# Optimization experiments

Measured on AMD Instinct MI355X. Metric: run time of the kernel, lower is better.

## Reference

```python
import jax, jax.numpy as jnp
import numpy as np

# Model constants (match init_kwargs)
H = 256          # hidden_dim
NH = 4           # num_heads
L = 4            # gnn_layers
T = 4            # transformer_layers
KMAX = 10        # k_max for overlap embedding
MAXD = 32        # MAX_DIST
INC = 119        # in_channels (atom vocab)
ED = 5           # edge_dim (bond vocab)
B = 64           # graphs per batch
M_SUB = 32       # subgraphs per graph (m)
KNODE = 32       # nodes per subgraph (k)
S = B * M_SUB    # total subgraphs = 2048
N = S * KNODE    # flattened nodes = 65536
E = 131072       # intra-subgraph directed edges


def _ln(x, g, b):
    mu = x.mean(-1, keepdims=True)
    var = ((x - mu) ** 2).mean(-1, keepdims=True)
    return (x - mu) * jax.lax.rsqrt(var + 1e-5) * g + b


def setup_inputs() -> dict:
    key = jax.random.key(0)
    ks = iter(jax.random.split(key, 24))
    nk = lambda: next(ks)
    rn = lambda k_, shp: 0.02 * jax.random.normal(k_, shp, dtype=jnp.float32)

    x_ids = jax.random.randint(nk(), (N,), 0, INC)
    edge_ids = jax.random.randint(nk(), (E,), 0, ED)
    # intra-subgraph edges: endpoints stay within each block of KNODE nodes
    eps_per = E // S
    base = jnp.repeat(jnp.arange(S) * KNODE, eps_per)
    src = base + jax.random.randint(nk(), (E,), 0, KNODE)
    dst = base + jax.random.randint(nk(), (E,), 0, KNODE)
    ns = jax.random.randint(nk(), (S, KNODE), 0, 500)
    padm = jax.random.uniform(nk(), (S, KNODE)) < 0.1
    nodes_sampled = jnp.where(padm, -1, ns)
    dist = jax.random.randint(nk(), (N,), 0, MAXD + 1)
    lp = -5.0 * jax.random.uniform(nk(), (S,))

    return {
        'x_ids': x_ids, 'edge_ids': edge_ids, 'src': src, 'dst': dst,
        'nodes_sampled': nodes_sampled, 'dist': dist, 'lp': lp,
        'atom_emb': rn(nk(), (INC, H)), 'bond_emb': rn(nk(), (ED, H)),
        'dist_emb': rn(nk(), (MAXD + 1, H)),
        'logp_W': rn(nk(), (H,)), 'logp_b': jnp.zeros((H,)),
        'gnn_eps': jnp.zeros((L,)),
        'gnn_W1': rn(nk(), (L, H, H)), 'gnn_b1': jnp.zeros((L, H)),
        'gnn_W2': rn(nk(), (L, H, H)), 'gnn_b2': jnp.zeros((L, H)),
        'ln1_g': jnp.ones((T, H)), 'ln1_b': jnp.zeros((T, H)),
        'qkv_W': rn(nk(), (T, H, 3 * H)),
        'out_W': rn(nk(), (T, H, H)), 'out_b': jnp.zeros((T, H)),
        'ln2_g': jnp.ones((T, H)), 'ln2_b': jnp.zeros((T, H)),
        'f1_W': rn(nk(), (T, H, 4 * H)), 'f1_b': jnp.zeros((T, 4 * H)),
        'f2_W': rn(nk(), (T, 4 * H, H)), 'f2_b': jnp.zeros((T, H)),
        'lnout_g': jnp.ones((H,)), 'lnout_b': jnp.zeros((H,)),
        'overlap_emb': rn(nk(), (KMAX + 1,)),
        'ht_alpha': jnp.ones(()),
    }


def reference(x_ids, edge_ids, src, dst, nodes_sampled, dist, lp,
              atom_emb, bond_emb, dist_emb, logp_W, logp_b,
              gnn_eps, gnn_W1, gnn_b1, gnn_W2, gnn_b2,
              ln1_g, ln1_b, qkv_W, out_W, out_b, ln2_g, ln2_b,
              f1_W, f1_b, f2_W, f2_b, lnout_g, lnout_b,
              overlap_emb, ht_alpha):
    # ---- flatten / embed node features ----
    valid = (nodes_sampled >= 0).reshape(N)
    valid_f = valid.astype(jnp.float32)[:, None]
    lp = jnp.where(jnp.isfinite(lp), lp, 0.0)
    sub_batch = jnp.arange(N) // KNODE
    dist_c = jnp.clip(dist, 0, MAXD)
    logp_pe = jax.nn.relu(lp[sub_batch][:, None] * logp_W + logp_b)
    h = (atom_emb[x_ids] + dist_emb[dist_c] + logp_pe) * valid_f  # [N,H]
    e = bond_emb[edge_ids]                                        # [E,H]

    # ---- GINE message passing ----
    for l in range(L):
        msg = jax.nn.relu(h[src] + e)                       # [E,H] gather
        agg = jax.ops.segment_sum(msg, dst, num_segments=N) # [N,H] scatter-add
        z = (1.0 + gnn_eps[l]) * h + agg
        z = jax.nn.relu(z @ gnn_W1[l] + gnn_b1[l])
        h = (z @ gnn_W2[l] + gnn_b2[l]) * valid_f

    # ---- pool roots into [B, m, H] tokens ----
    root = jnp.arange(S) * KNODE
    x = h[root].reshape(B, M_SUB, H)
    lp2 = lp.reshape(B, M_SUB)

    # ---- pairwise subgraph overlap bias ----
    nodes = nodes_sampled.reshape(B, M_SUB, KNODE)
    vmask = nodes >= 0
    # eq[b,i,j,ki,kj]: node ki of subgraph i equals node kj of subgraph j
    eq = nodes[:, :, None, :, None] == nodes[:, None, :, None, :]
    overlap = (eq.any(-1) & vmask[:, :, None, :]).sum(-1)  # [B,m,m]
    lp_c = jnp.clip(lp2, -30.0, 0.0)
    bias = overlap_emb[jnp.clip(overlap, 0, KMAX)] - ht_alpha * lp_c[:, None, :]
    bias = bias[:, None]  # [B,1,m,m], broadcast over heads

    # ---- relative-bias transformer ----
    hd = H // NH
    scale = 1.0 / np.sqrt(hd).astype(np.float32)
    for t in range(T):
        r = _ln(x, ln1_g[t], ln1_b[t])
        q, k_, v = jnp.split(r @ qkv_W[t], 3, axis=-1)
        q = q.reshape(B, M_SUB, NH, hd)
        k_ = k_.reshape(B, M_SUB, NH, hd)
        v = v.reshape(B, M_SUB, NH, hd)
        scores = jnp.einsum('bihd,bjhd->bhij', q, k_) * scale + bias
        attn = jax.nn.softmax(scores, axis=-1)
        o = jnp.einsum('bhij,bjhd->bihd', attn, v).reshape(B, M_SUB, H)
        x = x + o @ out_W[t] + out_b[t]
        r2 = _ln(x, ln2_g[t], ln2_b[t])
        x = x + jax.nn.gelu(r2 @ f1_W[t] + f1_b[t], approximate=False) @ f2_W[t] + f2_b[t]

    x = _ln(x, lnout_g, lnout_b)
    # HT-weighted mean over subgraph tokens
    w = jax.nn.softmax(-lp_c, axis=1)
    return (w[:, :, None] * x).sum(1)  # [B,H]
```

## Files before the change

kernel.cpp:

```cpp
#include <hip/hip_runtime.h>
#include <hip/hip_bf16.h>
#include <math.h>

#define HDIM   256
#define NHEAD  4
#define LLAY   4
#define TLAY   4
#define KMAXC  10
#define MAXD   32
#define BATCH  64
#define MSUB   32
#define KNODE  32
#define SSUB   2048
#define NNODE  65536
#define NEDGE  131072
#define EPSPER 64
#define EDN    5

typedef unsigned short u16;
typedef __attribute__((ext_vector_type(8))) short bf16x8;
typedef __attribute__((ext_vector_type(4))) float f32x4;

__device__ __forceinline__ float us2f(u16 u) {
    union { unsigned int i; float f; } x; x.i = ((unsigned int)u) << 16; return x.f;
}
__device__ __forceinline__ u16 f2us(float v) {
    union { float f; unsigned int i; } x; x.f = v;
    unsigned int u = x.i;
    u += 0x7fffu + ((u >> 16) & 1u);
    return (u16)(u >> 16);
}
__device__ __forceinline__ float finite_or_zero(float v) {
    return (v == v && fabsf(v) <= 3.0e38f) ? v : 0.0f;
}
__device__ __forceinline__ void gll16(const u16* g, u16* l) {
    __builtin_amdgcn_global_load_lds(
        (const __attribute__((address_space(1))) unsigned int*)g,
        (__attribute__((address_space(3))) unsigned int*)l, 16, 0, 0);
}

__global__ __launch_bounds__(256) void k_csr(
    const int* __restrict__ src, const int* __restrict__ dst,
    const int* __restrict__ eid, u16* __restrict__ perm, u16* __restrict__ off)
{
    __shared__ int sL[4][64], dL[4][64], eL[4][64];
    int wave = threadIdx.x >> 6, lane = threadIdx.x & 63;
    int sgi = blockIdx.x * 4 + wave;
    sL[wave][lane] = src[sgi * 64 + lane] - sgi * KNODE;
    dL[wave][lane] = dst[sgi * 64 + lane] - sgi * KNODE;
    eL[wave][lane] = eid[sgi * 64 + lane];
    __syncthreads();
    if (lane < 32) {
        int cnt = 0;
        for (int e = 0; e < 64; ++e) cnt += (dL[wave][e] == lane) ? 1 : 0;
        int incl = cnt;
        #pragma unroll
        for (int d = 1; d < 32; d <<= 1) {
            int v = __shfl_up(incl, d, 64);
            if (lane >= d) incl += v;
        }
        int start = incl - cnt;
        off[sgi * 32 + lane] = (u16)start;
        int pos = start;
        for (int e = 0; e < 64; ++e) {
            if (dL[wave][e] == lane) {
                perm[sgi * 64 + pos] = (u16)((sL[wave][e] << 3) | eL[wave][e]);
                ++pos;
            }
        }
    }
}

__global__ __launch_bounds__(256) void k_wtrans(
    const float* __restrict__ W, u16* __restrict__ WT, int K, int N)
{
    __shared__ float til[32][33];
    int k0 = blockIdx.x * 32, n0 = blockIdx.y * 32, s = blockIdx.z;
    const float* Wb = W + (size_t)s * K * N;
    u16* Tb = WT + (size_t)s * N * K;
    int j = threadIdx.x & 31, i0 = threadIdx.x >> 5;
    #pragma unroll
    for (int it = 0; it < 4; ++it) {
        int i = i0 + it * 8;
        til[i][j] = Wb[(size_t)(k0 + i) * N + n0 + j];
    }
    __syncthreads();
    #pragma unroll
    for (int it = 0; it < 4; ++it) {
        int i = i0 + it * 8;
        Tb[(size_t)(n0 + i) * K + k0 + j] = f2us(til[j][i]);
    }
}

__global__ __launch_bounds__(256, 4) void k_gnn4(
    const int* __restrict__ x_ids, const int* __restrict__ dist,
    const int* __restrict__ nodes, const float* __restrict__ lp,
    const float* __restrict__ atom_emb, const float* __restrict__ dist_emb,
    const float* __restrict__ logp_W, const float* __restrict__ logp_b,
    const u16* __restrict__ perm, const u16* __restrict__ off,
    const float* __restrict__ bond_emb, const float* __restrict__ eps_arr,
    const float* __restrict__ b1a, const float* __restrict__ b2a,
    const u16* __restrict__ W1T, const u16* __restrict__ W2T,
    float* __restrict__ x)
{
    __shared__ __align__(16) unsigned char smem[38912];
    u16*   hz    = (u16*)smem;
    float* bondL = (float*)(smem + 32768);
    u16*   permL = (u16*)(smem + 32768 + 5120);
    u16*   offL  = (u16*)(smem + 32768 + 5120 + 256);
    float* validL= (float*)(smem + 32768 + 5120 + 512);
    float* epsL  = (float*)(smem + 32768 + 5120 + 512 + 256);

    int tid = threadIdx.x, lane = tid & 63, wave = tid >> 6;
    int row0 = blockIdx.x * 64;
    int fr = lane & 15, quad = lane >> 4;

    for (int i = tid; i < EDN * 256; i += 256) bondL[i] = bond_emb[i];
    if (tid < 128) permL[tid] = perm[blockIdx.x * 128 + tid];
    if (tid < 64) {
        offL[tid] = off[blockIdx.x * 64 + tid];
        validL[tid] = (nodes[row0 + tid] >= 0) ? 1.0f : 0.0f;
    }
    if (tid < 4) epsL[tid] = eps_arr[tid];

    {
        int m = tid & 63, qd = tid >> 6;
        int rg = row0 + m;
        float valid = (nodes[rg] >= 0) ? 1.0f : 0.0f;
        float lpv = finite_or_zero(lp[rg >> 5]);
        int dc = dist[rg]; dc = dc < 0 ? 0 : (dc > MAXD ? MAXD : dc);
        int xid = x_ids[rg];
        #pragma unroll
        for (int k = 0; k < 8; ++k) {
            int cc = qd * 8 + k, c = cc * 8;
            float4 a0 = *reinterpret_cast<const float4*>(atom_emb + xid * 256 + c);
            float4 a1 = *reinterpret_cast<const float4*>(atom_emb + xid * 256 + c + 4);
            float4 d0 = *reinterpret_cast<const float4*>(dist_emb + dc * 256 + c);
            float4 d1 = *reinterpret_cast<const float4*>(dist_emb + dc * 256 + c + 4);
            float4 w0 = *reinterpret_cast<const float4*>(logp_W + c);
            float4 w1 = *reinterpret_cast<const float4*>(logp_W + c + 4);
            float4 p0 = *reinterpret_cast<const float4*>(logp_b + c);
            float4 p1 = *reinterpret_cast<const float4*>(logp_b + c + 4);
            union { bf16x8 v; ushort4 h[2]; } o;
            o.h[0] = (ushort4){
                f2us((a0.x + d0.x + fmaxf(lpv * w0.x + p0.x, 0.f)) * valid),
                f2us((a0.y + d0.y + fmaxf(lpv * w0.y + p0.y, 0.f)) * valid),
                f2us((a0.z + d0.z + fmaxf(lpv * w0.z + p0.z, 0.f)) * valid),
                f2us((a0.w + d0.w + fmaxf(lpv * w0.w + p0.w, 0.f)) * valid) };
            o.h[1] = (ushort4){
                f2us((a1.x + d1.x + fmaxf(lpv * w1.x + p1.x, 0.f)) * valid),
                f2us((a1.y + d1.y + fmaxf(lpv * w1.y + p1.y, 0.f)) * valid),
                f2us((a1.z + d1.z + fmaxf(lpv * w1.z + p1.z, 0.f)) * valid),
                f2us((a1.w + d1.w + fmaxf(lpv * w1.w + p1.w, 0.f)) * valid) };
            *reinterpret_cast<bf16x8*>(hz + m * 256 + ((cc ^ (m & 7)) * 8)) = o.v;
        }
    }
    __syncthreads();

    int rl = tid >> 3, g8 = tid & 7;
    for (int l = 0; l < LLAY; ++l) {
        float ep1 = 1.0f + epsL[l];
        for (int p = 0; p < 2; ++p) {
            int row = p * 32 + rl;
            int e0 = offL[p * 32 + rl];
            int e1 = (rl < 31) ? offL[p * 32 + rl + 1] : 64;
            float a[32];
            #pragma unroll
            for (int q = 0; q < 32; ++q) a[q] = 0.f;
            for (int j = e0; j < e1; ++j) {
                int ent = permL[p * 64 + j];
                int sl = p * 32 + (ent >> 3);
                int be = ent & 7;
                #pragma unroll
                for (int q = 0; q < 4; ++q) {
                    union { bf16x8 v; u16 s[8]; } hv;
                    hv.v = *reinterpret_cast<const bf16x8*>(
                        hz + sl * 256 + (((g8 * 4 + q) ^ (sl & 7)) * 8));
                    const float* bp = bondL + be * 256 + g8 * 32 + q * 8;
                    float4 bo0 = *reinterpret_cast<const float4*>(bp);
                    float4 bo1 = *reinterpret_cast<const float4*>(bp + 4);
                    a[q*8+0] += fmaxf(us2f(hv.s[0]) + bo0.x, 0.f);
                    a[q*8+1] += fmaxf(us2f(hv.s[1]) + bo0.y, 0.f);
                    a[q*8+2] += fmaxf(us2f(hv.s[2]) + bo0.z, 0.f);
                    a[q*8+3] += fmaxf(us2f(hv.s[3]) + bo0.w, 0.f);
                    a[q*8+4] += fmaxf(us2f(hv.s[4]) + bo1.x, 0.f);
                    a[q*8+5] += fmaxf(us2f(hv.s[5]) + bo1.y, 0.f);
                    a[q*8+6] += fmaxf(us2f(hv.s[6]) + bo1.z, 0.f);
                    a[q*8+7] += fmaxf(us2f(hv.s[7]) + bo1.w, 0.f);
                }
            }
            __syncthreads();
            #pragma unroll
            for (int q = 0; q < 4; ++q) {
                u16* ptr = hz + row * 256 + (((g8 * 4 + q) ^ (row & 7)) * 8);
                union { bf16x8 v; u16 s[8]; } hv, ov;
                hv.v = *reinterpret_cast<const bf16x8*>(ptr);
                #pragma unroll
                for (int k = 0; k < 8; ++k)
                    ov.s[k] = f2us(ep1 * us2f(hv.s[k]) + a[q * 8 + k]);
                *reinterpret_cast<bf16x8*>(ptr) = ov.v;
            }
        }
        __syncthreads();

        const u16* W1 = W1T + l * 65536;
        const float* b1 = b1a + l * 256;
        bf16x8 wf[4][8];
        #pragma unroll
        for (int i = 0; i < 4; ++i)
            #pragma unroll
            for (int kc = 0; kc < 8; ++kc)
                wf[i][kc] = *reinterpret_cast<const bf16x8*>(
                    W1 + (size_t)(wave * 64 + i * 16 + fr) * 256 + kc * 32 + quad * 8);
        f32x4 acc[4][4];
        #pragma unroll
        for (int i = 0; i < 4; ++i)
            #pragma unroll
            for (int j = 0; j < 4; ++j) acc[i][j] = (f32x4){0.f, 0.f, 0.f, 0.f};
        #pragma unroll
        for (int kc = 0; kc < 8; ++kc) {
            bf16x8 bfv[4];
            #pragma unroll
            for (int j = 0; j < 4; ++j) {
                int m = j * 16 + fr;
                bfv[j] = *reinterpret_cast<const bf16x8*>(hz + m * 256 + (((kc * 4 + quad) ^ (m & 7)) * 8));
            }
            #pragma unroll
            for (int i = 0; i < 4; ++i)
                #pragma unroll
                for (int j = 0; j < 4; ++j)
                    acc[i][j] = __builtin_amdgcn_mfma_f32_16x16x32_bf16(wf[i][kc], bfv[j], acc[i][j], 0, 0, 0);
        }
        __syncthreads();
        #pragma unroll
        for (int i = 0; i < 4; ++i) {
            int n1b = wave * 64 + i * 16 + quad * 4;
            float4 bb = *reinterpret_cast<const float4*>(b1 + n1b);
            #pragma unroll
            for (int j = 0; j < 4; ++j) {
                int m = j * 16 + fr;
                ushort4 o = { f2us(fmaxf(acc[i][j][0] + bb.x, 0.f)),
                              f2us(fmaxf(acc[i][j][1] + bb.y, 0.f)),
                              f2us(fmaxf(acc[i][j][2] + bb.z, 0.f)),
                              f2us(fmaxf(acc[i][j][3] + bb.w, 0.f)) };
                *reinterpret_cast<ushort4*>(hz + m * 256 + (((n1b >> 3) ^ (m & 7)) * 8) + (n1b & 7)) = o;
            }
        }
        __syncthreads();

        const u16* W2 = W2T + l * 65536;
        const float* b2 = b2a + l * 256;
        #pragma unroll
        for (int i = 0; i < 4; ++i)
            #pragma unroll
            for (int kc = 0; kc < 8; ++kc)
                wf[i][kc] = *reinterpret_cast<const bf16x8*>(
                    W2 + (size_t)(wave * 64 + i * 16 + fr) * 256 + kc * 32 + quad * 8);
        #pragma unroll
        for (int i = 0; i < 4; ++i)
            #pragma unroll
            for (int j = 0; j < 4; ++j) acc[i][j] = (f32x4){0.f, 0.f, 0.f, 0.f};
        #pragma unroll
        for (int kc = 0; kc < 8; ++kc) {
            bf16x8 bfv[4];
            #pragma unroll
            for (int j = 0; j < 4; ++j) {
                int m = j * 16 + fr;
                bfv[j] = *reinterpret_cast<const bf16x8*>(hz + m * 256 + (((kc * 4 + quad) ^ (m & 7)) * 8));
            }
            #pragma unroll
            for (int i = 0; i < 4; ++i)
                #pragma unroll
                for (int j = 0; j < 4; ++j)
                    acc[i][j] = __builtin_amdgcn_mfma_f32_16x16x32_bf16(wf[i][kc], bfv[j], acc[i][j], 0, 0, 0);
        }
        __syncthreads();

        if (l < LLAY - 1) {
            #pragma unroll
            for (int i = 0; i < 4; ++i) {
                int n2b = wave * 64 + i * 16 + quad * 4;
                float4 bb = *reinterpret_cast<const float4*>(b2 + n2b);
                #pragma unroll
                for (int j = 0; j < 4; ++j) {
                    int m = j * 16 + fr;
                    float vm = validL[m];
                    ushort4 o = { f2us((acc[i][j][0] + bb.x) * vm),
                                  f2us((acc[i][j][1] + bb.y) * vm),
                                  f2us((acc[i][j][2] + bb.z) * vm),
                                  f2us((acc[i][j][3] + bb.w) * vm) };
                    *reinterpret_cast<ushort4*>(hz + m * 256 + (((n2b >> 3) ^ (m & 7)) * 8) + (n2b & 7)) = o;
                }
            }
            __syncthreads();
        } else {
            if (fr == 0) {
                #pragma unroll
                for (int i = 0; i < 4; ++i) {
                    int n2b = wave * 64 + i * 16 + quad * 4;
                    float4 bb = *reinterpret_cast<const float4*>(b2 + n2b);
                    #pragma unroll
                    for (int jj = 0; jj < 2; ++jj) {
                        int j = jj * 2, m = j * 16;
                        float vm = validL[m];
                        float4 o = { (acc[i][j][0] + bb.x) * vm,
                                     (acc[i][j][1] + bb.y) * vm,
                                     (acc[i][j][2] + bb.z) * vm,
                                     (acc[i][j][3] + bb.w) * vm };
                        *reinterpret_cast<float4*>(
                            x + (size_t)(blockIdx.x * 2 + (m >> 5)) * 256 + n2b) = o;
                    }
                }
            }
        }
    }
}

__global__ __launch_bounds__(256) void k_tgemm64(
    const u16* __restrict__ A, const u16* __restrict__ BT,
    const float* __restrict__ bias, void* __restrict__ Cout, int c_is_bf16,
    const float* __restrict__ resid, const int* __restrict__ valid,
    int M, int K, int N, int act)
{
    __shared__ __align__(16) u16 As[2][64 * 32];
    __shared__ __align__(16) u16 Bs[2][64 * 32];
    int tid = threadIdx.x, lane = tid & 63, wave = tid >> 6;
    int wm = wave >> 1, wn = wave & 1;
    int bm = blockIdx.y * 64, bn = blockIdx.x * 64;
    const u16* gA = A + (size_t)(bm + wave * 16 + (lane >> 2)) * K + (lane & 3) * 8;
    const u16* gB = BT + (size_t)(bn + wave * 16 + (lane >> 2)) * K + (lane & 3) * 8;
    gll16(gA, &As[0][wave * 512]);
    gll16(gB, &Bs[0][wave * 512]);
    f32x4 acc[2][2];
    #pragma unroll
    for (int i = 0; i < 2; ++i)
        #pragma unroll
        for (int j = 0; j < 2; ++j) acc[i][j] = (f32x4){0.f, 0.f, 0.f, 0.f};
    int fr = lane & 15, quad = lane >> 4;
    int nit = K >> 5;
    __syncthreads();
    for (int it = 0; it < nit; ++it) {
        int buf = it & 1;
        if (it + 1 < nit) {
            int k0 = (it + 1) * 32;
            gll16(gA + k0, &As[buf ^ 1][wave * 512]);
            gll16(gB + k0, &Bs[buf ^ 1][wave * 512]);
        }
        bf16x8 af[2], bfr[2];
        #pragma unroll
        for (int i = 0; i < 2; ++i)
            af[i] = *reinterpret_cast<const bf16x8*>(&As[buf][(wm * 32 + i * 16 + fr) * 32 + quad * 8]);
        #pragma unroll
        for (int j = 0; j < 2; ++j)
            bfr[j] = *reinterpret_cast<const bf16x8*>(&Bs[buf][(wn * 32 + j * 16 + fr) * 32 + quad * 8]);
        #pragma unroll
        for (int i = 0; i < 2; ++i)
            #pragma unroll
            for (int j = 0; j < 2; ++j)
                acc[i][j] = __builtin_amdgcn_mfma_f32_16x16x32_bf16(af[i], bfr[j], acc[i][j], 0, 0, 0);
        __syncthreads();
    }
    int crow0 = bm + wm * 32 + quad * 4;
    int ccol0 = bn + wn * 32 + fr;
    #pragma unroll
    for (int i = 0; i < 2; ++i) {
        #pragma unroll
        for (int r = 0; r < 4; ++r) {
            int m = crow0 + i * 16 + r;
            float vm = valid ? ((valid[m] >= 0) ? 1.0f : 0.0f) : 1.0f;
            #pragma unroll
            for (int j = 0; j < 2; ++j) {
                int n = ccol0 + j * 16;
                float v = acc[i][j][r];
                if (bias) v += bias[n];
                if (act == 1) v = v > 0.f ? v : 0.f;
                else if (act == 2) v = 0.5f * v * (1.0f + erff(v * 0.70710678118654752f));
                v *= vm;
                if (resid) v += resid[(size_t)m * N + n];
                if (c_is_bf16) ((u16*)Cout)[(size_t)m * N + n] = f2us(v);
                else ((float*)Cout)[(size_t)m * N + n] = v;
            }
        }
    }
}

__global__ __launch_bounds__(256) void k_ln(
    const float* __restrict__ X, u16* __restrict__ Out,
    const float* __restrict__ g, const float* __restrict__ b)
{
    int row = blockIdx.x * 4 + (threadIdx.x >> 6);
    int lane = threadIdx.x & 63;
    float4 xv = *reinterpret_cast<const float4*>(X + (size_t)row * HDIM + lane * 4);
    float s = xv.x + xv.y + xv.z + xv.w;
    #pragma unroll
    for (int off = 32; off > 0; off >>= 1) s += __shfl_xor(s, off);
    float mu = s * (1.0f / HDIM);
    float d0 = xv.x - mu, d1 = xv.y - mu, d2 = xv.z - mu, d3 = xv.w - mu;
    float sq = d0 * d0 + d1 * d1 + d2 * d2 + d3 * d3;
    #pragma unroll
    for (int off = 32; off > 0; off >>= 1) sq += __shfl_xor(sq, off);
    float rs = rsqrtf(sq * (1.0f / HDIM) + 1e-5f);
    int c = lane * 4;
    float4 gv = *reinterpret_cast<const float4*>(g + c);
    float4 bv = *reinterpret_cast<const float4*>(b + c);
    ushort4 o = { f2us(d0 * rs * gv.x + bv.x), f2us(d1 * rs * gv.y + bv.y),
                  f2us(d2 * rs * gv.z + bv.z), f2us(d3 * rs * gv.w + bv.w) };
    *reinterpret_cast<ushort4*>(Out + (size_t)row * HDIM + c) = o;
}

__global__ __launch_bounds__(1024) void k_bias(
    const int* __restrict__ nodes, const float* __restrict__ lp,
    const float* __restrict__ ovl_emb, const float* __restrict__ alpha_p,
    float* __restrict__ bias)
{
    int b = blockIdx.x, tid = threadIdx.x;
    __shared__ int nd[32][32];
    __shared__ unsigned int bmv[32][17];
    __shared__ float lpc[32];
    __shared__ float emb[16];
    nd[tid >> 5][tid & 31] = nodes[b * 1024 + tid];
    if (tid < 512) bmv[tid >> 4][tid & 15] = 0u;
    if (tid < 32) {
        float l = finite_or_zero(lp[b * 32 + tid]);
        l = l < -30.f ? -30.f : (l > 0.f ? 0.f : l);
        lpc[tid] = l;
    }
    if (tid >= 64 && tid < 64 + KMAXC + 1) emb[tid - 64] = ovl_emb[tid - 64];
    __syncthreads();
    int own = nd[tid >> 5][tid & 31];
    if (own >= 0) atomicOr(&bmv[tid >> 5][own >> 5], 1u << (own & 31));
    __syncthreads();
    int i = tid >> 5, j = tid & 31;
    float alpha = alpha_p[0];
    int cnt = 0;
    #pragma unroll
    for (int k = 0; k < 32; ++k) {
        int nk = nd[i][k];
        if (nk >= 0) cnt += (int)((bmv[j][nk >> 5] >> (nk & 31)) & 1u);
    }
    bias[b * 1024 + tid] = emb[cnt > KMAXC ? KMAXC : cnt] - alpha * lpc[j];
}

__global__ __launch_bounds__(256) void k_attn(
    const u16* __restrict__ qkv, const float* __restrict__ bias, u16* __restrict__ o)
{
    int b = blockIdx.x >> 2, hh = blockIdx.x & 3;
    __shared__ float qs[32][65], ks[32][65], vs[32][65];
    __shared__ float sc[32][33];
    int tid = threadIdx.x;
    #pragma unroll
    for (int u = 0; u < 8; ++u) {
        int idx = tid + u * 256;
        int i = idx >> 6, d = idx & 63;
        size_t base = (size_t)(b * 32 + i) * 768;
        qs[i][d] = us2f(qkv[base + hh * 64 + d]);
        ks[i][d] = us2f(qkv[base + 256 + hh * 64 + d]);
        vs[i][d] = us2f(qkv[base + 512 + hh * 64 + d]);
    }
    __syncthreads();
    #pragma unroll
    for (int u = 0; u < 4; ++u) {
        int p = tid + u * 256;
        int i = p >> 5, j = p & 31;
        float s = 0.f;
        #pragma unroll
        for (int d = 0; d < 64; ++d) s += qs[i][d] * ks[j][d];
        sc[i][j] = s * 0.125f + bias[b * 1024 + i * 32 + j];
    }
    __syncthreads();
    if (tid < 32) {
        int i = tid;
        float m = -1e30f;
        for (int j = 0; j < 32; ++j) m = fmaxf(m, sc[i][j]);
        float sum = 0.f;
        for (int j = 0; j < 32; ++j) { float e = expf(sc[i][j] - m); sc[i][j] = e; sum += e; }
        float inv = 1.0f / sum;
        for (int j = 0; j < 32; ++j) sc[i][j] *= inv;
    }
    __syncthreads();
    #pragma unroll
    for (int u = 0; u < 8; ++u) {
        int idx = tid + u * 256;
        int i = idx >> 6, d = idx & 63;
        float a = 0.f;
        #pragma unroll
        for (int j = 0; j < 32; ++j) a += sc[i][j] * vs[j][d];
        o[(size_t)(b * 32 + i) * HDIM + hh * 64 + d] = f2us(a);
    }
}

__global__ __launch_bounds__(256) void k_final(
    const u16* __restrict__ xln, const float* __restrict__ lp, float* __restrict__ out)
{
    int b = blockIdx.x, tid = threadIdx.x;
    __shared__ float w[32];
    if (tid < 32) {
        float l = finite_or_zero(lp[b * 32 + tid]);
        l = l < -30.f ? -30.f : (l > 0.f ? 0.f : l);
        w[tid] = -l;
    }
    __syncthreads();
    if (tid == 0) {
        float m = -1e30f;
        for (int i = 0; i < 32; ++i) m = fmaxf(m, w[i]);
        float s = 0.f;
        for (int i = 0; i < 32; ++i) { float e = expf(w[i] - m); w[i] = e; s += e; }
        float inv = 1.0f / s;
        for (int i = 0; i < 32; ++i) w[i] *= inv;
    }
    __syncthreads();
    float acc = 0.f;
    for (int i = 0; i < 32; ++i) acc += w[i] * us2f(xln[(size_t)(b * 32 + i) * HDIM + tid]);
    out[b * HDIM + tid] = acc;
}

extern "C" void kernel_launch(void* const* d_in, const int* in_sizes, int n_in,
                              void* d_out, int out_size, void* d_ws, size_t ws_size,
                              hipStream_t stream)
{
    const int*   x_ids    = (const int*)d_in[0];
    const int*   edge_ids = (const int*)d_in[1];
    const int*   srcp     = (const int*)d_in[2];
    const int*   dstp     = (const int*)d_in[3];
    const int*   nodes    = (const int*)d_in[4];
    const int*   dist     = (const int*)d_in[5];
    const float* lp       = (const float*)d_in[6];
    const float* atom_emb = (const float*)d_in[7];
    const float* bond_emb = (const float*)d_in[8];
    const float* dist_emb = (const float*)d_in[9];
    const float* logp_W   = (const float*)d_in[10];
    const float* logp_b   = (const float*)d_in[11];
    const float* gnn_eps  = (const float*)d_in[12];
    const float* gnn_W1   = (const float*)d_in[13];
    const float* gnn_b1   = (const float*)d_in[14];
    const float* gnn_W2   = (const float*)d_in[15];
    const float* gnn_b2   = (const float*)d_in[16];
    const float* ln1_g    = (const float*)d_in[17];
    const float* ln1_b    = (const float*)d_in[18];
    const float* qkv_W    = (const float*)d_in[19];
    const float* out_W    = (const float*)d_in[20];
    const float* out_b    = (const float*)d_in[21];
    const float* ln2_g    = (const float*)d_in[22];
    const float* ln2_b    = (const float*)d_in[23];
    const float* f1_W     = (const float*)d_in[24];
    const float* f1_b     = (const float*)d_in[25];
    const float* f2_W     = (const float*)d_in[26];
    const float* f2_b     = (const float*)d_in[27];
    const float* lnout_g  = (const float*)d_in[28];
    const float* lnout_b  = (const float*)d_in[29];
    const float* ovl_emb  = (const float*)d_in[30];
    const float* alpha    = (const float*)d_in[31];

    char* ws = (char*)d_ws;
    u16*   gW1T  = (u16*)(ws + 100663296ull);
    u16*   gW2T  = (u16*)(ws + 100663296ull + 524288ull);
    u16*   permW = (u16*)(ws + 100663296ull + 1048576ull);
    u16*   offW  = (u16*)(ws + 100663296ull + 1310720ull);
    u16*   r     = (u16*)(ws + 33554432ull);
    u16*   ob    = (u16*)(ws + 33554432ull + 1048576ull);
    u16*   qkvb  = (u16*)(ws + 33554432ull + 2097152ull);
    u16*   ffh   = (u16*)(ws + 33554432ull + 5242880ull);
    u16*   xln   = (u16*)(ws + 33554432ull + 9437184ull);
    float* biasb = (float*)(ws + 33554432ull + 10485760ull);
    u16*   qkvT  = (u16*)(ws + 33554432ull + 11534336ull);
    u16*   outT  = (u16*)(ws + 33554432ull + 13107200ull);
    u16*   f1T   = (u16*)(ws + 33554432ull + 13631488ull);
    u16*   f2T   = (u16*)(ws + 33554432ull + 15728640ull);
    float* x     = (float*)(ws + 67108864ull);

    k_csr<<<SSUB / 4, 256, 0, stream>>>(srcp, dstp, edge_ids, permW, offW);
    k_wtrans<<<dim3(8, 8, 4), 256, 0, stream>>>(gnn_W1, gW1T, 256, 256);
    k_wtrans<<<dim3(8, 8, 4), 256, 0, stream>>>(gnn_W2, gW2T, 256, 256);
    k_gnn4<<<NNODE / 64, 256, 0, stream>>>(
        x_ids, dist, nodes, lp, atom_emb, dist_emb, logp_W, logp_b,
        permW, offW, bond_emb, gnn_eps, gnn_b1, gnn_b2, gW1T, gW2T, x);
    k_wtrans<<<dim3(8, 24, 4), 256, 0, stream>>>(qkv_W, qkvT, 256, 768);
    k_wtrans<<<dim3(8, 8, 4), 256, 0, stream>>>(out_W, outT, 256, 256);
    k_wtrans<<<dim3(8, 32, 4), 256, 0, stream>>>(f1_W, f1T, 256, 1024);
    k_wtrans<<<dim3(32, 8, 4), 256, 0, stream>>>(f2_W, f2T, 1024, 256);
    k_bias<<<BATCH, 1024, 0, stream>>>(nodes, lp, ovl_emb, alpha, biasb);
    for (int t = 0; t < TLAY; ++t) {
        k_ln<<<SSUB / 4, 256, 0, stream>>>(x, r, ln1_g + t * HDIM, ln1_b + t * HDIM);
        k_tgemm64<<<dim3(12, SSUB / 64), 256, 0, stream>>>(
            r, qkvT + t * 768 * 256, nullptr, qkvb, 1,
            nullptr, nullptr, SSUB, 256, 768, 0);
        k_attn<<<BATCH * NHEAD, 256, 0, stream>>>(qkvb, biasb, ob);
        k_tgemm64<<<dim3(4, SSUB / 64), 256, 0, stream>>>(
            ob, outT + t * 65536, out_b + t * HDIM, x, 0,
            x, nullptr, SSUB, 256, HDIM, 0);
        k_ln<<<SSUB / 4, 256, 0, stream>>>(x, r, ln2_g + t * HDIM, ln2_b + t * HDIM);
        k_tgemm64<<<dim3(16, SSUB / 64), 256, 0, stream>>>(
            r, f1T + t * 1024 * 256, f1_b + t * 1024, ffh, 1,
            nullptr, nullptr, SSUB, 256, 1024, 2);
        k_tgemm64<<<dim3(4, SSUB / 64), 256, 0, stream>>>(
            ffh, f2T + t * 256 * 1024, f2_b + t * HDIM, x, 0,
            x, nullptr, SSUB, 1024, HDIM, 0);
    }
    k_ln<<<SSUB / 4, 256, 0, stream>>>(x, xln, lnout_g, lnout_b);
    k_final<<<BATCH, 256, 0, stream>>>(xln, lp, (float*)d_out);
}
```

Baseline: 587.1 us.

## Fuse entire transformer stack into one per-graph persistent kernel

```diff
diff --git a/kernel.cpp b/kernel.cpp
--- a/kernel.cpp
+++ b/kernel.cpp
@@ -92,7 +92,7 @@
     }
 }
 
-__global__ __launch_bounds__(256, 4) void k_gnn4(
+__global__ __launch_bounds__(256, 2) void k_gnn4(
     const int* __restrict__ x_ids, const int* __restrict__ dist,
     const int* __restrict__ nodes, const float* __restrict__ lp,
     const float* __restrict__ atom_emb, const float* __restrict__ dist_emb,
@@ -316,202 +316,387 @@
     }
 }
 
-__global__ __launch_bounds__(256) void k_tgemm64(
-    const u16* __restrict__ A, const u16* __restrict__ BT,
-    const float* __restrict__ bias, void* __restrict__ Cout, int c_is_bf16,
-    const float* __restrict__ resid, const int* __restrict__ valid,
-    int M, int K, int N, int act)
+#define TF_XF    0
+#define TF_RB    33280
+#define TF_BIAS  49664
+#define TF_LPC   53888
+#define TF_WFIN  54016
+#define TF_EMB   54144
+#define TF_U     54272
+#define TF_QKV   54272
+#define TF_QS    103424
+#define TF_KS    111744
+#define TF_VS    120064
+#define TF_SC    128384
+#define TF_OB    132608
+#define TF_FFH   54272
+#define TF_XLN   54272
+#define XSTR 260
+__global__ __launch_bounds__(256, 1) void k_tformer(
+    const float* __restrict__ x, const int* __restrict__ nodes,
+    const float* __restrict__ lp, const float* __restrict__ ovl_emb,
+    const float* __restrict__ alpha_p,
+    const float* __restrict__ ln1_g, const float* __restrict__ ln1_b,
+    const u16* __restrict__ qkvT, const u16* __restrict__ outT,
+    const float* __restrict__ out_b,
+    const float* __restrict__ ln2_g, const float* __restrict__ ln2_b,
+    const u16* __restrict__ f1T, const float* __restrict__ f1_b,
+    const u16* __restrict__ f2T, const float* __restrict__ f2_b,
+    const float* __restrict__ lnout_g, const float* __restrict__ lnout_b,
+    float* __restrict__ out)
 {
-    __shared__ __align__(16) u16 As[2][64 * 32];
-    __shared__ __align__(16) u16 Bs[2][64 * 32];
+    __shared__ __align__(16) unsigned char smem[148992];
+    float* xf   = (float*)(smem + TF_XF);
+    u16*   rb   = (u16*)(smem + TF_RB);
+    float* biasL= (float*)(smem + TF_BIAS);
+    float* lpc  = (float*)(smem + TF_LPC);
+    float* wfin = (float*)(smem + TF_WFIN);
+    float* emb  = (float*)(smem + TF_EMB);
+    u16*   qkvb = (u16*)(smem + TF_QKV);
+    float* qs   = (float*)(smem + TF_QS);
+    float* ks   = (float*)(smem + TF_KS);
+    float* vs   = (float*)(smem + TF_VS);
+    float* sc   = (float*)(smem + TF_SC);
+    u16*   obL  = (u16*)(smem + TF_OB);
+    u16*   ffh  = (u16*)(smem + TF_FFH);
+    float* xlnf = (float*)(smem + TF_XLN);
+
     int tid = threadIdx.x, lane = tid & 63, wave = tid >> 6;
-    int wm = wave >> 1, wn = wave & 1;
-    int bm = blockIdx.y * 64, bn = blockIdx.x * 64;
-    const u16* gA = A + (size_t)(bm + wave * 16 + (lane >> 2)) * K + (lane & 3) * 8;
-    const u16* gB = BT + (size_t)(bn + wave * 16 + (lane >> 2)) * K + (lane & 3) * 8;
-    gll16(gA, &As[0][wave * 512]);
-    gll16(gB, &Bs[0][wave * 512]);
-    f32x4 acc[2][2];
-    #pragma unroll
-    for (int i = 0; i < 2; ++i)
-        #pragma unroll
-        for (int j = 0; j < 2; ++j) acc[i][j] = (f32x4){0.f, 0.f, 0.f, 0.f};
+    int b = blockIdx.x;
     int fr = lane & 15, quad = lane >> 4;
-    int nit = K >> 5;
-    __syncthreads();
-    for (int it = 0; it < nit; ++it) {
-        int buf = it & 1;
-        if (it + 1 < nit) {
-            int k0 = (it + 1) * 32;
-            gll16(gA + k0, &As[buf ^ 1][wave * 512]);
-            gll16(gB + k0, &Bs[buf ^ 1][wave * 512]);
-        }
-        bf16x8 af[2], bfr[2];
-        #pragma unroll
-        for (int i = 0; i < 2; ++i)
-            af[i] = *reinterpret_cast<const bf16x8*>(&As[buf][(wm * 32 + i * 16 + fr) * 32 + quad * 8]);
-        #pragma unroll
-        for (int j = 0; j < 2; ++j)
-            bfr[j] = *reinterpret_cast<const bf16x8*>(&Bs[buf][(wn * 32 + j * 16 + fr) * 32 + quad * 8]);
-        #pragma unroll
-        for (int i = 0; i < 2; ++i)
-            #pragma unroll
-            for (int j = 0; j < 2; ++j)
-                acc[i][j] = __builtin_amdgcn_mfma_f32_16x16x32_bf16(af[i], bfr[j], acc[i][j], 0, 0, 0);
-        __syncthreads();
-    }
-    int crow0 = bm + wm * 32 + quad * 4;
-    int ccol0 = bn + wn * 32 + fr;
-    #pragma unroll
-    for (int i = 0; i < 2; ++i) {
-        #pragma unroll
-        for (int r = 0; r < 4; ++r) {
-            int m = crow0 + i * 16 + r;
-            float vm = valid ? ((valid[m] >= 0) ? 1.0f : 0.0f) : 1.0f;
-            #pragma unroll
-            for (int j = 0; j < 2; ++j) {
-                int n = ccol0 + j * 16;
-                float v = acc[i][j][r];
-                if (bias) v += bias[n];
-                if (act == 1) v = v > 0.f ? v : 0.f;
-                else if (act == 2) v = 0.5f * v * (1.0f + erff(v * 0.70710678118654752f));
-                v *= vm;
-                if (resid) v += resid[(size_t)m * N + n];
-                if (c_is_bf16) ((u16*)Cout)[(size_t)m * N + n] = f2us(v);
-                else ((float*)Cout)[(size_t)m * N + n] = v;
-            }
-        }
-    }
-}
-
-__global__ __launch_bounds__(256) void k_ln(
-    const float* __restrict__ X, u16* __restrict__ Out,
-    const float* __restrict__ g, const float* __restrict__ b)
-{
-    int row = blockIdx.x * 4 + (threadIdx.x >> 6);
-    int lane = threadIdx.x & 63;
-    float4 xv = *reinterpret_cast<const float4*>(X + (size_t)row * HDIM + lane * 4);
-    float s = xv.x + xv.y + xv.z + xv.w;
-    #pragma unroll
-    for (int off = 32; off > 0; off >>= 1) s += __shfl_xor(s, off);
-    float mu = s * (1.0f / HDIM);
-    float d0 = xv.x - mu, d1 = xv.y - mu, d2 = xv.z - mu, d3 = xv.w - mu;
-    float sq = d0 * d0 + d1 * d1 + d2 * d2 + d3 * d3;
-    #pragma unroll
-    for (int off = 32; off > 0; off >>= 1) sq += __shfl_xor(sq, off);
-    float rs = rsqrtf(sq * (1.0f / HDIM) + 1e-5f);
-    int c = lane * 4;
-    float4 gv = *reinterpret_cast<const float4*>(g + c);
-    float4 bv = *reinterpret_cast<const float4*>(b + c);
-    ushort4 o = { f2us(d0 * rs * gv.x + bv.x), f2us(d1 * rs * gv.y + bv.y),
-                  f2us(d2 * rs * gv.z + bv.z), f2us(d3 * rs * gv.w + bv.w) };
-    *reinterpret_cast<ushort4*>(Out + (size_t)row * HDIM + c) = o;
-}
-
-__global__ __launch_bounds__(1024) void k_bias(
-    const int* __restrict__ nodes, const float* __restrict__ lp,
-    const float* __restrict__ ovl_emb, const float* __restrict__ alpha_p,
-    float* __restrict__ bias)
-{
-    int b = blockIdx.x, tid = threadIdx.x;
-    __shared__ int nd[32][32];
-    __shared__ unsigned int bmv[32][17];
-    __shared__ float lpc[32];
-    __shared__ float emb[16];
-    nd[tid >> 5][tid & 31] = nodes[b * 1024 + tid];
-    if (tid < 512) bmv[tid >> 4][tid & 15] = 0u;
-    if (tid < 32) {
-        float l = finite_or_zero(lp[b * 32 + tid]);
-        l = l < -30.f ? -30.f : (l > 0.f ? 0.f : l);
-        lpc[tid] = l;
-    }
-    if (tid >= 64 && tid < 64 + KMAXC + 1) emb[tid - 64] = ovl_emb[tid - 64];
-    __syncthreads();
-    int own = nd[tid >> 5][tid & 31];
-    if (own >= 0) atomicOr(&bmv[tid >> 5][own >> 5], 1u << (own & 31));
-    __syncthreads();
-    int i = tid >> 5, j = tid & 31;
-    float alpha = alpha_p[0];
-    int cnt = 0;
-    #pragma unroll
-    for (int k = 0; k < 32; ++k) {
-        int nk = nd[i][k];
-        if (nk >= 0) cnt += (int)((bmv[j][nk >> 5] >> (nk & 31)) & 1u);
-    }
-    bias[b * 1024 + tid] = emb[cnt > KMAXC ? KMAXC : cnt] - alpha * lpc[j];
-}
-
-__global__ __launch_bounds__(256) void k_attn(
-    const u16* __restrict__ qkv, const float* __restrict__ bias, u16* __restrict__ o)
-{
-    int b = blockIdx.x >> 2, hh = blockIdx.x & 3;
-    __shared__ float qs[32][65], ks[32][65], vs[32][65];
-    __shared__ float sc[32][33];
-    int tid = threadIdx.x;
+
     #pragma unroll
     for (int u = 0; u < 8; ++u) {
-        int idx = tid + u * 256;
-        int i = idx >> 6, d = idx & 63;
-        size_t base = (size_t)(b * 32 + i) * 768;
-        qs[i][d] = us2f(qkv[base + hh * 64 + d]);
-        ks[i][d] = us2f(qkv[base + 256 + hh * 64 + d]);
-        vs[i][d] = us2f(qkv[base + 512 + hh * 64 + d]);
+        int v = u * 256 + tid;
+        int i = v >> 6, c = (v & 63) * 4;
+        *reinterpret_cast<float4*>(xf + i * XSTR + c) =
+            *reinterpret_cast<const float4*>(x + (size_t)(b * 32 + i) * 256 + c);
+    }
+    {
+        int* nd = (int*)(smem + TF_U);
+        unsigned int* bmv = (unsigned int*)(smem + TF_U + 4096);
+        #pragma unroll
+        for (int u = 0; u < 4; ++u) nd[tid + u * 256] = nodes[b * 1024 + tid + u * 256];
+        for (int i = tid; i < 544; i += 256) bmv[i] = 0u;
+        if (tid < 32) {
+            float l = finite_or_zero(lp[b * 32 + tid]);
+            l = l < -30.f ? -30.f : (l > 0.f ? 0.f : l);
+            lpc[tid] = l;
+        }
+        if (tid <= KMAXC) emb[tid] = ovl_emb[tid];
+        __syncthreads();
+        #pragma unroll
+        for (int u = 0; u < 4; ++u) {
+            int p = tid + u * 256;
+            int own = nd[p];
+            if (own >= 0) atomicOr(&bmv[(p >> 5) * 17 + (own >> 5)], 1u << (own & 31));
+        }
+        __syncthreads();
+        float alpha = alpha_p[0];
+        #pragma unroll
+        for (int u = 0; u < 4; ++u) {
+            int p = tid + u * 256;
+            int i = p >> 5, j = p & 31;
+            int cnt = 0;
+            #pragma unroll
+            for (int k = 0; k < 32; ++k) {
+                int nk = nd[i * 32 + k];
+                if (nk >= 0) cnt += (int)((bmv[j * 17 + (nk >> 5)] >> (nk & 31)) & 1u);
+            }
+            biasL[i * 33 + j] = emb[cnt > KMAXC ? KMAXC : cnt] - alpha * lpc[j];
+        }
     }
     __syncthreads();
+
+    for (int t = 0; t < TLAY; ++t) {
+        {
+            const float* g = ln1_g + t * 256;
+            const float* bb = ln1_b + t * 256;
+            #pragma unroll
+            for (int rr = 0; rr < 8; ++rr) {
+                int row = wave * 8 + rr;
+                float4 xv = *reinterpret_cast<const float4*>(xf + row * XSTR + lane * 4);
+                float s = xv.x + xv.y + xv.z + xv.w;
+                #pragma unroll
+                for (int o2 = 32; o2 > 0; o2 >>= 1) s += __shfl_xor(s, o2);
+                float mu = s * (1.0f / 256.0f);
+                float d0 = xv.x - mu, d1 = xv.y - mu, d2 = xv.z - mu, d3 = xv.w - mu;
+                float sq = d0 * d0 + d1 * d1 + d2 * d2 + d3 * d3;
+                #pragma unroll
+                for (int o2 = 32; o2 > 0; o2 >>= 1) sq += __shfl_xor(sq, o2);
+                float rs = rsqrtf(sq * (1.0f / 256.0f) + 1e-5f);
+                int c = lane * 4;
+                float4 gv = *reinterpret_cast<const float4*>(g + c);
+                float4 bv = *reinterpret_cast<const float4*>(bb + c);
+                ushort4 o = { f2us(d0 * rs * gv.x + bv.x), f2us(d1 * rs * gv.y + bv.y),
+                              f2us(d2 * rs * gv.z + bv.z), f2us(d3 * rs * gv.w + bv.w) };
+                *reinterpret_cast<ushort4*>(rb + row * 256 + (((c >> 3) ^ (row & 7)) * 8) + (c & 7)) = o;
+            }
+        }
+        __syncthreads();
+        {
+            const u16* W = qkvT + (size_t)t * 768 * 256;
+            f32x4 acc[12][2];
+            #pragma unroll
+            for (int i = 0; i < 12; ++i) { acc[i][0] = (f32x4){0,0,0,0}; acc[i][1] = (f32x4){0,0,0,0}; }
+            for (int kc = 0; kc < 8; ++kc) {
+                bf16x8 wf[12], bfv[2];
+                #pragma unroll
+                for (int i = 0; i < 12; ++i)
+                    wf[i] = *reinterpret_cast<const bf16x8*>(
+                        W + (size_t)((wave * 12 + i) * 16 + fr) * 256 + kc * 32 + quad * 8);
+                #pragma unroll
+                for (int j = 0; j < 2; ++j) {
+                    int m = j * 16 + fr;
+                    bfv[j] = *reinterpret_cast<const bf16x8*>(rb + m * 256 + (((kc * 4 + quad) ^ (m & 7)) * 8));
+                }
+                #pragma unroll
+                for (int i = 0; i < 12; ++i)
+                    #pragma unroll
+                    for (int j = 0; j < 2; ++j)
+                        acc[i][j] = __builtin_amdgcn_mfma_f32_16x16x32_bf16(wf[i], bfv[j], acc[i][j], 0, 0, 0);
+            }
+            __syncthreads();
+            #pragma unroll
+            for (int i = 0; i < 12; ++i) {
+                int n1b = (wave * 12 + i) * 16 + quad * 4;
+                #pragma unroll
+                for (int j = 0; j < 2; ++j) {
+                    int m = j * 16 + fr;
+                    ushort4 o = { f2us(acc[i][j][0]), f2us(acc[i][j][1]),
+                                  f2us(acc[i][j][2]), f2us(acc[i][j][3]) };
+                    *reinterpret_cast<ushort4*>(qkvb + m * 768 + (((n1b >> 3) ^ (m & 7)) * 8) + (n1b & 7)) = o;
+                }
+            }
+        }
+        __syncthreads();
+        for (int hh = 0; hh < NHEAD; ++hh) {
+            #pragma unroll
+            for (int u = 0; u < 8; ++u) {
+                int idx = tid + u * 256;
+                int i = idx >> 6, d = idx & 63;
+                int cq = hh * 64 + d, ck = 256 + hh * 64 + d, cv = 512 + hh * 64 + d;
+                qs[i * 65 + d] = us2f(qkvb[i * 768 + (((cq >> 3) ^ (i & 7)) * 8) + (cq & 7)]);
+                ks[i * 65 + d] = us2f(qkvb[i * 768 + (((ck >> 3) ^ (i & 7)) * 8) + (ck & 7)]);
+                vs[i * 65 + d] = us2f(qkvb[i * 768 + (((cv >> 3) ^ (i & 7)) * 8) + (cv & 7)]);
+            }
+            __syncthreads();
+            #pragma unroll
+            for (int u = 0; u < 4; ++u) {
+                int p = tid + u * 256;
+                int i = p >> 5, j = p & 31;
+                float s = 0.f;
+                #pragma unroll
+                for (int d = 0; d < 64; ++d) s += qs[i * 65 + d] * ks[j * 65 + d];
+                sc[i * 33 + j] = s * 0.125f + biasL[i * 33 + j];
+            }
+            __syncthreads();
+            if (tid < 32) {
+                int i = tid;
+                float m = -1e30f;
+                for (int j = 0; j < 32; ++j) m = fmaxf(m, sc[i * 33 + j]);
+                float sum = 0.f;
+                for (int j = 0; j < 32; ++j) { float e = expf(sc[i * 33 + j] - m); sc[i * 33 + j] = e; sum += e; }
+                float inv = 1.0f / sum;
+                for (int j = 0; j < 32; ++j) sc[i * 33 + j] *= inv;
+            }
+            __syncthreads();
+            #pragma unroll
+            for (int u = 0; u < 8; ++u) {
+                int idx = tid + u * 256;
+                int i = idx >> 6, d = idx & 63;
+                float a = 0.f;
+                #pragma unroll
+                for (int j = 0; j < 32; ++j) a += sc[i * 33 + j] * vs[j * 65 + d];
+                int c = hh * 64 + d;
+                obL[i * 256 + (((c >> 3) ^ (i & 7)) * 8) + (c & 7)] = f2us(a);
+            }
+            __syncthreads();
+        }
+        {
+            const u16* W = outT + (size_t)t * 65536;
+            const float* bb = out_b + t * 256;
+            f32x4 acc[4][2];
+            #pragma unroll
+            for (int i = 0; i < 4; ++i) { acc[i][0] = (f32x4){0,0,0,0}; acc[i][1] = (f32x4){0,0,0,0}; }
+            for (int kc = 0; kc < 8; ++kc) {
+                bf16x8 wf[4], bfv[2];
+                #pragma unroll
+                for (int i = 0; i < 4; ++i)
+                    wf[i] = *reinterpret_cast<const bf16x8*>(
+                        W + (size_t)((wave * 4 + i) * 16 + fr) * 256 + kc * 32 + quad * 8);
+                #pragma unroll
+                for (int j = 0; j < 2; ++j) {
+                    int m = j * 16 + fr;
+                    bfv[j] = *reinterpret_cast<const bf16x8*>(obL + m * 256 + (((kc * 4 + quad) ^ (m & 7)) * 8));
+                }
+                #pragma unroll
+                for (int i = 0; i < 4; ++i)
+                    #pragma unroll
+                    for (int j = 0; j < 2; ++j)
+                        acc[i][j] = __builtin_amdgcn_mfma_f32_16x16x32_bf16(wf[i], bfv[j], acc[i][j], 0, 0, 0);
+            }
+            __syncthreads();
+            #pragma unroll
+            for (int i = 0; i < 4; ++i) {
+                int n1b = (wave * 4 + i) * 16 + quad * 4;
+                float4 bv = *reinterpret_cast<const float4*>(bb + n1b);
+                #pragma unroll
+                for (int j = 0; j < 2; ++j) {
+                    int m = j * 16 + fr;
+                    float4* px = reinterpret_cast<float4*>(xf + m * XSTR + n1b);
+                    float4 xv = *px;
+                    xv.x += acc[i][j][0] + bv.x; xv.y += acc[i][j][1] + bv.y;
+                    xv.z += acc[i][j][2] + bv.z; xv.w += acc[i][j][3] + bv.w;
+                    *px = xv;
+                }
+            }
+        }
+        __syncthreads();
+        {
+            const float* g = ln2_g + t * 256;
+            const float* bb = ln2_b + t * 256;
+            #pragma unroll
+            for (int rr = 0; rr < 8; ++rr) {
+                int row = wave * 8 + rr;
+                float4 xv = *reinterpret_cast<const float4*>(xf + row * XSTR + lane * 4);
+                float s = xv.x + xv.y + xv.z + xv.w;
+                #pragma unroll
+                for (int o2 = 32; o2 > 0; o2 >>= 1) s += __shfl_xor(s, o2);
+                float mu = s * (1.0f / 256.0f);
+                float d0 = xv.x - mu, d1 = xv.y - mu, d2 = xv.z - mu, d3 = xv.w - mu;
+                float sq = d0 * d0 + d1 * d1 + d2 * d2 + d3 * d3;
+                #pragma unroll
+                for (int o2 = 32; o2 > 0; o2 >>= 1) sq += __shfl_xor(sq, o2);
+                float rs = rsqrtf(sq * (1.0f / 256.0f) + 1e-5f);
+                int c = lane * 4;
+                float4 gv = *reinterpret_cast<const float4*>(g + c);
+                float4 bv = *reinterpret_cast<const float4*>(bb + c);
+                ushort4 o = { f2us(d0 * rs * gv.x + bv.x), f2us(d1 * rs * gv.y + bv.y),
+                              f2us(d2 * rs * gv.z + bv.z), f2us(d3 * rs * gv.w + bv.w) };
+                *reinterpret_cast<ushort4*>(rb + row * 256 + (((c >> 3) ^ (row & 7)) * 8) + (c & 7)) = o;
+            }
+        }
+        __syncthreads();
+        {
+            const u16* W = f1T + (size_t)t * 1024 * 256;
+            const float* bb = f1_b + t * 1024;
+            f32x4 acc[16][2];
+            #pragma unroll
+            for (int i = 0; i < 16; ++i) { acc[i][0] = (f32x4){0,0,0,0}; acc[i][1] = (f32x4){0,0,0,0}; }
+            for (int kc = 0; kc < 8; ++kc) {
+                bf16x8 wf[16], bfv[2];
+                #pragma unroll
+                for (int i = 0; i < 16; ++i)
+                    wf[i] = *reinterpret_cast<const bf16x8*>(
+                        W + (size_t)((wave * 16 + i) * 16 + fr) * 256 + kc * 32 + quad * 8);
+                #pragma unroll
+                for (int j = 0; j < 2; ++j) {
+                    int m = j * 16 + fr;
+                    bfv[j] = *reinterpret_cast<const bf16x8*>(rb + m * 256 + (((kc * 4 + quad) ^ (m & 7)) * 8));
+                }
+                #pragma unroll
+                for (int i = 0; i < 16; ++i)
+                    #pragma unroll
+                    for (int j = 0; j < 2; ++j)
+                        acc[i][j] = __builtin_amdgcn_mfma_f32_16x16x32_bf16(wf[i], bfv[j], acc[i][j], 0, 0, 0);
+            }
+            __syncthreads();
+            #pragma unroll
+            for (int i = 0; i < 16; ++i) {
+                int n1b = (wave * 16 + i) * 16 + quad * 4;
+                float4 bv = *reinterpret_cast<const float4*>(bb + n1b);
+                #pragma unroll
+                for (int j = 0; j < 2; ++j) {
+                    int m = j * 16 + fr;
+                    float v0 = acc[i][j][0] + bv.x, v1 = acc[i][j][1] + bv.y;
+                    float v2 = acc[i][j][2] + bv.z, v3 = acc[i][j][3] + bv.w;
+                    v0 = 0.5f * v0 * (1.0f + erff(v0 * 0.70710678118654752f));
+                    v1 = 0.5f * v1 * (1.0f + erff(v1 * 0.70710678118654752f));
+                    v2 = 0.5f * v2 * (1.0f + erff(v2 * 0.70710678118654752f));
+                    v3 = 0.5f * v3 * (1.0f + erff(v3 * 0.70710678118654752f));
+                    ushort4 o = { f2us(v0), f2us(v1), f2us(v2), f2us(v3) };
+                    *reinterpret_cast<ushort4*>(ffh + m * 1024 + (((n1b >> 3) ^ (m & 7)) * 8) + (n1b & 7)) = o;
+                }
+            }
+        }
+        __syncthreads();
+        {
+            const u16* W = f2T + (size_t)t * 256 * 1024;
+            const float* bb = f2_b + t * 256;
+            f32x4 acc[4][2];
+            #pragma unroll
+            for (int i = 0; i < 4; ++i) { acc[i][0] = (f32x4){0,0,0,0}; acc[i][1] = (f32x4){0,0,0,0}; }
+            for (int kc = 0; kc < 32; ++kc) {
+                bf16x8 wf[4], bfv[2];
+                #pragma unroll
+                for (int i = 0; i < 4; ++i)
+                    wf[i] = *reinterpret_cast<const bf16x8*>(
+                        W + (size_t)((wave * 4 + i) * 16 + fr) * 1024 + kc * 32 + quad * 8);
+                #pragma unroll
+                for (int j = 0; j < 2; ++j) {
+                    int m = j * 16 + fr;
+                    bfv[j] = *reinterpret_cast<const bf16x8*>(ffh + m * 1024 + (((kc * 4 + quad) ^ (m & 7)) * 8));
+                }
+                #pragma unroll
+                for (int i = 0; i < 4; ++i)
+                    #pragma unroll
+                    for (int j = 0; j < 2; ++j)
+                        acc[i][j] = __builtin_amdgcn_mfma_f32_16x16x32_bf16(wf[i], bfv[j], acc[i][j], 0, 0, 0);
+            }
+            __syncthreads();
+            #pragma unroll
+            for (int i = 0; i < 4; ++i) {
+                int n1b = (wave * 4 + i) * 16 + quad * 4;
+                float4 bv = *reinterpret_cast<const float4*>(bb + n1b);
+                #pragma unroll
+                for (int j = 0; j < 2; ++j) {
+                    int m = j * 16 + fr;
+                    float4* px = reinterpret_cast<float4*>(xf + m * XSTR + n1b);
+                    float4 xv = *px;
+                    xv.x += acc[i][j][0] + bv.x; xv.y += acc[i][j][1] + bv.y;
+                    xv.z += acc[i][j][2] + bv.z; xv.w += acc[i][j][3] + bv.w;
+                    *px = xv;
+                }
+            }
+        }
+        __syncthreads();
+    }
+
     #pragma unroll
-    for (int u = 0; u < 4; ++u) {
-        int p = tid + u * 256;
-        int i = p >> 5, j = p & 31;
-        float s = 0.f;
-        #pragma unroll
-        for (int d = 0; d < 64; ++d) s += qs[i][d] * ks[j][d];
-        sc[i][j] = s * 0.125f + bias[b * 1024 + i * 32 + j];
-    }
-    __syncthreads();
-    if (tid < 32) {
-        int i = tid;
-        float m = -1e30f;
-        for (int j = 0; j < 32; ++j) m = fmaxf(m, sc[i][j]);
-        float sum = 0.f;
-        for (int j = 0; j < 32; ++j) { float e = expf(sc[i][j] - m); sc[i][j] = e; sum += e; }
-        float inv = 1.0f / sum;
-        for (int j = 0; j < 32; ++j) sc[i][j] *= inv;
-    }
-    __syncthreads();
-    #pragma unroll
-    for (int u = 0; u < 8; ++u) {
-        int idx = tid + u * 256;
-        int i = idx >> 6, d = idx & 63;
-        float a = 0.f;
-        #pragma unroll
-        for (int j = 0; j < 32; ++j) a += sc[i][j] * vs[j][d];
-        o[(size_t)(b * 32 + i) * HDIM + hh * 64 + d] = f2us(a);
-    }
-}
-
-__global__ __launch_bounds__(256) void k_final(
-    const u16* __restrict__ xln, const float* __restrict__ lp, float* __restrict__ out)
-{
-    int b = blockIdx.x, tid = threadIdx.x;
-    __shared__ float w[32];
-    if (tid < 32) {
-        float l = finite_or_zero(lp[b * 32 + tid]);
-        l = l < -30.f ? -30.f : (l > 0.f ? 0.f : l);
-        w[tid] = -l;
-    }
-    __syncthreads();
+    for (int rr = 0; rr < 8; ++rr) {
+        int row = wave * 8 + rr;
+        float4 xv = *reinterpret_cast<const float4*>(xf + row * XSTR + lane * 4);
+        float s = xv.x + xv.y + xv.z + xv.w;
+        #pragma unroll
+        for (int o2 = 32; o2 > 0; o2 >>= 1) s += __shfl_xor(s, o2);
+        float mu = s * (1.0f / 256.0f);
+        float d0 = xv.x - mu, d1 = xv.y - mu, d2 = xv.z - mu, d3 = xv.w - mu;
+        float sq = d0 * d0 + d1 * d1 + d2 * d2 + d3 * d3;
+        #pragma unroll
+        for (int o2 = 32; o2 > 0; o2 >>= 1) sq += __shfl_xor(sq, o2);
+        float rs = rsqrtf(sq * (1.0f / 256.0f) + 1e-5f);
+        int c = lane * 4;
+        float4 gv = *reinterpret_cast<const float4*>(lnout_g + c);
+        float4 bv = *reinterpret_cast<const float4*>(lnout_b + c);
+        float4 o = { d0 * rs * gv.x + bv.x, d1 * rs * gv.y + bv.y,
+                     d2 * rs * gv.z + bv.z, d3 * rs * gv.w + bv.w };
+        *reinterpret_cast<float4*>(xlnf + row * XSTR + c) = o;
+    }
     if (tid == 0) {
         float m = -1e30f;
-        for (int i = 0; i < 32; ++i) m = fmaxf(m, w[i]);
+        for (int i = 0; i < 32; ++i) m = fmaxf(m, -lpc[i]);
         float s = 0.f;
-        for (int i = 0; i < 32; ++i) { float e = expf(w[i] - m); w[i] = e; s += e; }
+        for (int i = 0; i < 32; ++i) { float e = expf(-lpc[i] - m); wfin[i] = e; s += e; }
         float inv = 1.0f / s;
-        for (int i = 0; i < 32; ++i) w[i] *= inv;
+        for (int i = 0; i < 32; ++i) wfin[i] *= inv;
     }
     __syncthreads();
-    float acc = 0.f;
-    for (int i = 0; i < 32; ++i) acc += w[i] * us2f(xln[(size_t)(b * 32 + i) * HDIM + tid]);
-    out[b * HDIM + tid] = acc;
+    {
+        float a = 0.f;
+        for (int i = 0; i < 32; ++i) a += wfin[i] * xlnf[i * XSTR + tid];
+        out[(size_t)b * 256 + tid] = a;
+    }
 }
 
 extern "C" void kernel_launch(void* const* d_in, const int* in_sizes, int n_in,
@@ -556,16 +741,10 @@
     u16*   gW2T  = (u16*)(ws + 100663296ull + 524288ull);
     u16*   permW = (u16*)(ws + 100663296ull + 1048576ull);
     u16*   offW  = (u16*)(ws + 100663296ull + 1310720ull);
-    u16*   r     = (u16*)(ws + 33554432ull);
-    u16*   ob    = (u16*)(ws + 33554432ull + 1048576ull);
-    u16*   qkvb  = (u16*)(ws + 33554432ull + 2097152ull);
-    u16*   ffh   = (u16*)(ws + 33554432ull + 5242880ull);
-    u16*   xln   = (u16*)(ws + 33554432ull + 9437184ull);
-    float* biasb = (float*)(ws + 33554432ull + 10485760ull);
-    u16*   qkvT  = (u16*)(ws + 33554432ull + 11534336ull);
-    u16*   outT  = (u16*)(ws + 33554432ull + 13107200ull);
-    u16*   f1T   = (u16*)(ws + 33554432ull + 13631488ull);
-    u16*   f2T   = (u16*)(ws + 33554432ull + 15728640ull);
+    u16*   qkvT  = (u16*)(ws + 33554432ull);
+    u16*   outT  = (u16*)(ws + 33554432ull + 1572864ull);
+    u16*   f1T   = (u16*)(ws + 33554432ull + 2097152ull);
+    u16*   f2T   = (u16*)(ws + 33554432ull + 4194304ull);
     float* x     = (float*)(ws + 67108864ull);
 
     k_csr<<<SSUB / 4, 256, 0, stream>>>(srcp, dstp, edge_ids, permW, offW);
@@ -578,24 +757,8 @@
     k_wtrans<<<dim3(8, 8, 4), 256, 0, stream>>>(out_W, outT, 256, 256);
     k_wtrans<<<dim3(8, 32, 4), 256, 0, stream>>>(f1_W, f1T, 256, 1024);
     k_wtrans<<<dim3(32, 8, 4), 256, 0, stream>>>(f2_W, f2T, 1024, 256);
-    k_bias<<<BATCH, 1024, 0, stream>>>(nodes, lp, ovl_emb, alpha, biasb);
-    for (int t = 0; t < TLAY; ++t) {
-        k_ln<<<SSUB / 4, 256, 0, stream>>>(x, r, ln1_g + t * HDIM, ln1_b + t * HDIM);
-        k_tgemm64<<<dim3(12, SSUB / 64), 256, 0, stream>>>(
-            r, qkvT + t * 768 * 256, nullptr, qkvb, 1,
-            nullptr, nullptr, SSUB, 256, 768, 0);
-        k_attn<<<BATCH * NHEAD, 256, 0, stream>>>(qkvb, biasb, ob);
-        k_tgemm64<<<dim3(4, SSUB / 64), 256, 0, stream>>>(
-            ob, outT + t * 65536, out_b + t * HDIM, x, 0,
-            x, nullptr, SSUB, 256, HDIM, 0);
-        k_ln<<<SSUB / 4, 256, 0, stream>>>(x, r, ln2_g + t * HDIM, ln2_b + t * HDIM);
-        k_tgemm64<<<dim3(16, SSUB / 64), 256, 0, stream>>>(
-            r, f1T + t * 1024 * 256, f1_b + t * 1024, ffh, 1,
-            nullptr, nullptr, SSUB, 256, 1024, 2);
-        k_tgemm64<<<dim3(4, SSUB / 64), 256, 0, stream>>>(
-            ffh, f2T + t * 256 * 1024, f2_b + t * HDIM, x, 0,
-            x, nullptr, SSUB, 1024, HDIM, 0);
-    }
-    k_ln<<<SSUB / 4, 256, 0, stream>>>(x, xln, lnout_g, lnout_b);
-    k_final<<<BATCH, 256, 0, stream>>>(xln, lp, (float*)d_out);
-}
+    k_tformer<<<BATCH, 256, 0, stream>>>(
+        x, nodes, lp, ovl_emb, alpha,
+        ln1_g, ln1_b, qkvT, outT, out_b, ln2_g, ln2_b,
+        f1T, f1_b, f2T, f2_b, lnout_g, lnout_b, (float*)d_out);
+}
```

Result: slower. 885.5 us (+50.8%).
